# Performance work log

Hardware: AMD Instinct MI355X
Metric: run time of the kernel (lower is better)

The kernel has to match this reference:

```python
import jax, jax.numpy as jnp
import numpy as np

N = 100000      # nodes
E = 1600000     # edges (avg degree 16)
IN_FEATS = 128
HEADS = 4
OUT_FEATS = 16
NEG_SLOPE = 0.2
EPS = 1e-16


def setup_inputs() -> dict:
    key = jax.random.key(0)
    k1, k2, k3, k4, k5, k6 = jax.random.split(key, 6)
    feat = jax.random.normal(k1, (N, IN_FEATS), dtype=jnp.float32)
    # xavier-ish scale for params
    W = jax.random.normal(k2, (IN_FEATS, HEADS * OUT_FEATS), dtype=jnp.float32) * 0.1
    attn_l = jax.random.normal(k3, (1, HEADS, OUT_FEATS), dtype=jnp.float32) * 0.1
    attn_r = jax.random.normal(k4, (1, HEADS, OUT_FEATS), dtype=jnp.float32) * 0.1
    src_index = jax.random.randint(k5, (E,), 0, N, dtype=jnp.int32)
    trg_index = jax.random.randint(k6, (E,), 0, N, dtype=jnp.int32)
    return {"feat": feat, "W": W, "attn_l": attn_l, "attn_r": attn_r,
            "src_index": src_index, "trg_index": trg_index}


def reference(feat, W, attn_l, attn_r, src_index, trg_index):
    # dropout layers are identity in eval mode
    n = feat.shape[0]
    h = (feat @ W).reshape(n, HEADS, OUT_FEATS)            # [N,H,F]
    el = jnp.sum(h * attn_l, axis=-1)                      # [N,H]
    er = jnp.sum(h * attn_r, axis=-1)                      # [N,H]
    s = el[src_index] + er[trg_index]                      # [E,H] edge scores
    s = jnp.where(s > 0, s, NEG_SLOPE * s)                 # LeakyReLU(0.2)
    # neighborhood-aware softmax over incoming edges of each target node
    s = s - jnp.max(s)                                     # global max shift (as in source)
    e = jnp.exp(s)                                         # [E,H]
    denom = jax.ops.segment_sum(e, trg_index, num_segments=n)  # [N,H]
    attn = e / (denom[trg_index] + EPS)                    # [E,H]
    # weighted aggregation of lifted source features into target nodes
    msg = h[src_index] * attn[:, :, None]                  # [E,H,F]
    h_prime = jax.ops.segment_sum(msg, trg_index, num_segments=n)  # [N,H,F]
    return h_prime.reshape(n, HEADS * OUT_FEATS)
```

## Files before the change

kernel.cpp:

```cpp
#include <hip/hip_runtime.h>

typedef unsigned short ushort_t;
typedef __attribute__((ext_vector_type(8))) short bf16x8;
typedef __attribute__((ext_vector_type(4))) float f32x4v;

#define BN 128
#define LOGBN 7
#define CAP 3072
#define MAXBKT 1024
#define NB3 256

static __device__ __forceinline__ ushort_t f2bf(float f) {
  union { float f; unsigned int i; } v; v.f = f;
  unsigned int r = v.i + 0x7FFFu + ((v.i >> 16) & 1u);
  return (ushort_t)(r >> 16);
}
static __device__ __forceinline__ float leaky(float s) {
  return s > 0.f ? s : 0.2f * s;
}

__global__ __launch_bounds__(256) void packw_hist(
    const float* __restrict__ W, const float* __restrict__ attnl,
    const float* __restrict__ attnr, ushort_t* __restrict__ wfrag,
    const int* __restrict__ trg, int E, int nbkt,
    int* __restrict__ blockHist, int epb)
{
  const int b = blockIdx.x;
  const int t = threadIdx.x;
  if (b == NB3) {
    __shared__ float sW[128 * 64];
    __shared__ float sAl[64], sAr[64];
    for (int i = t; i < 128 * 64 / 4; i += 256)
      ((float4*)sW)[i] = ((const float4*)W)[i];
    if (t < 64) sAl[t] = attnl[t];
    else if (t < 128) sAr[t - 64] = attnr[t - 64];
    __syncthreads();
    const int kc = t >> 6, l = t & 63;
    const int q = l >> 4, n = l & 15;
    #pragma unroll
    for (int tile = 0; tile < 5; ++tile) {
      #pragma unroll
      for (int j = 0; j < 8; ++j) {
        const int k = kc * 32 + q * 8 + j;
        float v = 0.f;
        if (tile < 4) {
          v = sW[k * 64 + tile * 16 + n];
        } else if (n < 4) {
          for (int f = 0; f < 16; ++f)
            v += sW[k * 64 + n * 16 + f] * sAl[n * 16 + f];
        } else if (n < 8) {
          const int hd = n - 4;
          for (int f = 0; f < 16; ++f)
            v += sW[k * 64 + hd * 16 + f] * sAr[hd * 16 + f];
        }
        wfrag[((tile * 4 + kc) * 64 + l) * 8 + j] = f2bf(v);
      }
    }
    return;
  }
  __shared__ int hist[MAXBKT];
  for (int i = t; i < nbkt; i += 256) hist[i] = 0;
  __syncthreads();
  const int start = b * epb;
  const int end = min(start + epb, E);
  for (int e = start + t; e < end; e += 256)
    atomicAdd(&hist[trg[e] >> LOGBN], 1);
  __syncthreads();
  for (int i = t; i < nbkt; i += 256) blockHist[b * nbkt + i] = hist[i];
}

__global__ __launch_bounds__(256) void linear_scan(
    const float* __restrict__ feat, const ushort_t* __restrict__ wfrag,
    ushort_t* __restrict__ h_out, float* __restrict__ el, float* __restrict__ er,
    float* __restrict__ blockmax2, int N, int nbL,
    int* __restrict__ blockHist, int nbkt, int* __restrict__ colTotal)
{
  __shared__ ushort_t sFb[64 * 136];
  __shared__ float wmax[8];
  __shared__ int wt[4];
  const int t = threadIdx.x;
  const int b = blockIdx.x;
  const int w = t >> 6, l = t & 63;

  if (b >= nbL) {
    const int sb = b - nbL;
    const int v = blockHist[t * nbkt + sb];
    int incl = v;
    #pragma unroll
    for (int d = 1; d < 64; d <<= 1) {
      int u = __shfl_up(incl, d, 64);
      if (l >= d) incl += u;
    }
    if (l == 63) wt[w] = incl;
    __syncthreads();
    int woff = 0;
    for (int k = 0; k < w; ++k) woff += wt[k];
    blockHist[t * nbkt + sb] = woff + incl - v;
    if (t == 255) colTotal[sb] = woff + incl;
    return;
  }

  const int q = l >> 4, m = l & 15;
  const float4* gF = (const float4*)(feat + (size_t)b * 64 * 128);
  #pragma unroll
  for (int i = 0; i < 8; ++i) {
    const int idx = i * 256 + t;
    const int node = idx >> 5, off = idx & 31;
    float4 v = make_float4(0.f, 0.f, 0.f, 0.f);
    if (b * 64 + node < N) v = gF[idx];
    unsigned int p0 = ((unsigned int)f2bf(v.y) << 16) | f2bf(v.x);
    unsigned int p1 = ((unsigned int)f2bf(v.w) << 16) | f2bf(v.z);
    *(uint2*)(sFb + node * 136 + off * 4) = make_uint2(p0, p1);
  }
  __syncthreads();

  bf16x8 a[4];
  const ushort_t* arow = sFb + (w * 16 + m) * 136 + q * 8;
  #pragma unroll
  for (int kc = 0; kc < 4; ++kc)
    a[kc] = *(const bf16x8*)(arow + kc * 32);

  #pragma unroll
  for (int tile = 0; tile < 4; ++tile) {
    f32x4v acc = {0.f, 0.f, 0.f, 0.f};
    #pragma unroll
    for (int kc = 0; kc < 4; ++kc) {
      bf16x8 bfr = *(const bf16x8*)(wfrag + ((tile * 4 + kc) * 64 + l) * 8);
      acc = __builtin_amdgcn_mfma_f32_16x16x32_bf16(a[kc], bfr, acc, 0, 0, 0);
    }
    #pragma unroll
    for (int r = 0; r < 4; ++r) {
      const int gn = b * 64 + w * 16 + q * 4 + r;
      if (gn < N) h_out[(size_t)gn * 64 + tile * 16 + m] = f2bf(acc[r]);
    }
  }

  f32x4v acc4 = {0.f, 0.f, 0.f, 0.f};
  #pragma unroll
  for (int kc = 0; kc < 4; ++kc) {
    bf16x8 bfr = *(const bf16x8*)(wfrag + ((4 * 4 + kc) * 64 + l) * 8);
    acc4 = __builtin_amdgcn_mfma_f32_16x16x32_bf16(a[kc], bfr, acc4, 0, 0, 0);
  }
  float mel = -1e30f, mer = -1e30f;
  #pragma unroll
  for (int r = 0; r < 4; ++r) {
    const int gn = b * 64 + w * 16 + q * 4 + r;
    const float v = acc4[r];
    if (m < 4) {
      if (gn < N) el[gn * 4 + m] = v;
      mel = fmaxf(mel, v);
    } else if (m < 8) {
      if (gn < N) er[gn * 4 + (m - 4)] = v;
      mer = fmaxf(mer, v);
    }
  }
  #pragma unroll
  for (int o = 1; o <= 32; o <<= 1) {
    mel = fmaxf(mel, __shfl_xor(mel, o, 64));
    mer = fmaxf(mer, __shfl_xor(mer, o, 64));
  }
  if (l == 0) { wmax[w * 2] = mel; wmax[w * 2 + 1] = mer; }
  __syncthreads();
  if (t == 0) {
    float aa = fmaxf(fmaxf(wmax[0], wmax[2]), fmaxf(wmax[4], wmax[6]));
    float cc = fmaxf(fmaxf(wmax[1], wmax[3]), fmaxf(wmax[5], wmax[7]));
    blockmax2[b * 2] = aa;
    blockmax2[b * 2 + 1] = cc;
  }
}

__global__ __launch_bounds__(256) void bucket_scatter(
    const int* __restrict__ src, const int* __restrict__ trg, int E, int nbkt,
    const int* __restrict__ blockHist, const int* __restrict__ colTotal,
    unsigned int* __restrict__ binned, int epb, int* __restrict__ bucketBase)
{
  __shared__ int cursor[MAXBKT];
  __shared__ int wt[4];
  const int t = threadIdx.x, b = blockIdx.x;
  const int l = t & 63, w = t >> 6;

  int carry = 0;
  for (int ch = 0; ch * 256 < nbkt; ++ch) {
    const int i = ch * 256 + t;
    const int v = (i < nbkt) ? colTotal[i] : 0;
    int incl = v;
    #pragma unroll
    for (int d = 1; d < 64; d <<= 1) {
      int u = __shfl_up(incl, d, 64);
      if (l >= d) incl += u;
    }
    if (l == 63) wt[w] = incl;
    __syncthreads();
    int woff = 0;
    for (int k = 0; k < w; ++k) woff += wt[k];
    if (i < nbkt) cursor[i] = carry + woff + incl - v;
    carry += wt[0] + wt[1] + wt[2] + wt[3];
    __syncthreads();
  }
  if (b == 0) {
    for (int i = t; i < nbkt; i += 256) bucketBase[i] = cursor[i];
    if (t == 0) bucketBase[nbkt] = carry;
  }
  for (int i = t; i < nbkt; i += 256) cursor[i] += blockHist[b * nbkt + i];
  __syncthreads();

  const int start = b * epb;
  const int end = min(start + epb, E);
  for (int e = start + t; e < end; e += 256) {
    const int ti = trg[e];
    const int bkt = ti >> LOGBN;
    const int pos = atomicAdd(&cursor[bkt], 1);
    binned[pos] = ((unsigned int)src[e] << LOGBN) | (unsigned int)(ti & (BN - 1));
  }
}

__global__ __launch_bounds__(256) void fine_sort(
    unsigned int* __restrict__ binned, const int* __restrict__ bucketBase,
    int* __restrict__ rowbeg, int* __restrict__ rowend, int N,
    const float* __restrict__ blockmax2, int nbL, float* __restrict__ gmaxM)
{
  __shared__ unsigned int pld[CAP];
  __shared__ int hist[BN];
  __shared__ int cursor[BN];
  __shared__ int wtot[2];
  __shared__ float wmg[8];
  const int t = threadIdx.x;
  const int b = blockIdx.x;
  const int base = bucketBase[b];
  const int cn = min(bucketBase[b + 1] - base, CAP);
  unsigned int* slot = binned + base;

  if (t < BN) hist[t] = 0;
  if (b == 0) {
    const int l = t & 63, w = t >> 6;
    float mel = -1e30f, mer = -1e30f;
    for (int i = t; i < nbL; i += 256) {
      mel = fmaxf(mel, blockmax2[i * 2]);
      mer = fmaxf(mer, blockmax2[i * 2 + 1]);
    }
    #pragma unroll
    for (int o = 1; o <= 32; o <<= 1) {
      mel = fmaxf(mel, __shfl_xor(mel, o, 64));
      mer = fmaxf(mer, __shfl_xor(mer, o, 64));
    }
    if (l == 0) { wmg[w * 2] = mel; wmg[w * 2 + 1] = mer; }
  }
  __syncthreads();
  if (b == 0 && t == 0) {
    float aa = fmaxf(fmaxf(wmg[0], wmg[2]), fmaxf(wmg[4], wmg[6]));
    float cc = fmaxf(fmaxf(wmg[1], wmg[3]), fmaxf(wmg[5], wmg[7]));
    gmaxM[0] = fmaxf(0.f, aa + cc);
  }
  for (int i = t; i < cn; i += 256) {
    const unsigned int pv = slot[i];
    pld[i] = pv;
    atomicAdd(&hist[pv & (BN - 1)], 1);
  }
  __syncthreads();

  int v = 0, incl = 0;
  if (t < BN) {
    v = hist[t];
    incl = v;
    #pragma unroll
    for (int d = 1; d < 64; d <<= 1) {
      int u = __shfl_up(incl, d, 64);
      if ((t & 63) >= d) incl += u;
    }
  }
  if (t < BN && (t & 63) == 63) wtot[t >> 6] = incl;
  __syncthreads();
  if (t < BN) {
    const int excl = incl - v + ((t >= 64) ? wtot[0] : 0);
    cursor[t] = excl;
    const int node = b * BN + t;
    if (node < N) {
      rowbeg[node] = base + excl;
      rowend[node] = base + excl + v;
    }
  }
  __syncthreads();

  for (int i = t; i < cn; i += 256) {
    const unsigned int pv = pld[i];
    const int pos = atomicAdd(&cursor[pv & (BN - 1)], 1);
    slot[pos] = pv >> LOGBN;
  }
}

#define UNPACK_FMA(hv, p, acc) do { \
  union { unsigned int i; float f; } c_; \
  c_.i = (hv).x << 16;          acc[0] += c_.f * (p); \
  c_.i = (hv).x & 0xffff0000u;  acc[1] += c_.f * (p); \
  c_.i = (hv).y << 16;          acc[2] += c_.f * (p); \
  c_.i = (hv).y & 0xffff0000u;  acc[3] += c_.f * (p); \
  c_.i = (hv).z << 16;          acc[4] += c_.f * (p); \
  c_.i = (hv).z & 0xffff0000u;  acc[5] += c_.f * (p); \
  c_.i = (hv).w << 16;          acc[6] += c_.f * (p); \
  c_.i = (hv).w & 0xffff0000u;  acc[7] += c_.f * (p); \
} while (0)

#define LOADJ(j, hA_, hB_, qA_, qB_) do { \
  const int i_ = iA0 + (j) * 4; \
  const int sA_ = sSw[i_]; \
  const int sB_ = sSw[i_ + 32]; \
  qA_ = sPw[i_ * 4 + hd2]; \
  qB_ = sPw[(i_ + 32) * 4 + hd2]; \
  hA_ = *(const uint4*)(hcg + (size_t)sA_ * 64); \
  hB_ = *(const uint4*)(hcg + (size_t)sB_ * 64); \
} while (0)

__global__ __launch_bounds__(256) void gat_agg(
    const unsigned int* __restrict__ csrsrc, const int* __restrict__ rowbeg,
    const int* __restrict__ rowend,
    const float4* __restrict__ el4, const float4* __restrict__ er4,
    const ushort_t* __restrict__ hbf, const float* __restrict__ gmaxM,
    float* __restrict__ out, int N)
{
  __shared__ float sP[4 * 64 * 4];
  __shared__ int sS[4 * 64];
  const int t = threadIdx.x;
  const int l = t & 63;
  const int w = t >> 6;
  const int nbase = blockIdx.x * 16 + w * 4;
  const int rg = l >> 3;
  const int cg = l & 7;
  const int hd2 = cg >> 1;
  const int ks = l >> 4;
  const int le = l & 15;
  const float M = gmaxM[0];
  float* sPw = sP + w * 256;
  int* sSw = sS + w * 64;
  const ushort_t* hcg = hbf + cg * 8;
  const int iA0 = ((rg >> 2) * 16) + (rg & 3);

  const int nk = nbase + ks;
  int rs = 0, re = 0;
  if (nk < N) { rs = rowbeg[nk]; re = rowend[nk]; }
  const float4 ernk = (rs < re) ? er4[nk]
                                : make_float4(0.f, 0.f, 0.f, 0.f);
  int deg = re - rs;
  deg = max(deg, __shfl_xor(deg, 16, 64));
  deg = max(deg, __shfl_xor(deg, 32, 64));
  const int chunks = (deg + 15) >> 4;

  float aA[8] = {0.f,0.f,0.f,0.f,0.f,0.f,0.f,0.f};
  float aB[8] = {0.f,0.f,0.f,0.f,0.f,0.f,0.f,0.f};
  float dA = 0.f, dB = 0.f;

  for (int c = 0; c < chunks; ++c) {
    int sn = 0;
    float4 pv = make_float4(0.f, 0.f, 0.f, 0.f);
    const int ei = rs + c * 16 + le;
    if (ei < re) {
      sn = (int)csrsrc[ei];
      const float4 a = el4[sn];
      pv.x = __expf(leaky(a.x + ernk.x) - M);
      pv.y = __expf(leaky(a.y + ernk.y) - M);
      pv.z = __expf(leaky(a.z + ernk.z) - M);
      pv.w = __expf(leaky(a.w + ernk.w) - M);
    }
    *(float4*)(sPw + l * 4) = pv;
    sSw[l] = sn;

    const int rem = min(deg - c * 16, 16);
    const int jmax = (rem + 3) >> 2;
    uint4 h0A, h0B, h1A, h1B, h2A, h2B, h3A, h3B;
    float q0A, q0B, q1A, q1B, q2A, q2B, q3A, q3B;
    LOADJ(0, h0A, h0B, q0A, q0B);
    if (jmax > 1) LOADJ(1, h1A, h1B, q1A, q1B);
    if (jmax > 2) LOADJ(2, h2A, h2B, q2A, q2B);
    if (jmax > 3) LOADJ(3, h3A, h3B, q3A, q3B);

    UNPACK_FMA(h0A, q0A, aA); UNPACK_FMA(h0B, q0B, aB);
    dA += q0A; dB += q0B;
    if (jmax > 1) {
      UNPACK_FMA(h1A, q1A, aA); UNPACK_FMA(h1B, q1B, aB);
      dA += q1A; dB += q1B;
    }
    if (jmax > 2) {
      UNPACK_FMA(h2A, q2A, aA); UNPACK_FMA(h2B, q2B, aB);
      dA += q2A; dB += q2B;
    }
    if (jmax > 3) {
      UNPACK_FMA(h3A, q3A, aA); UNPACK_FMA(h3B, q3B, aB);
      dA += q3A; dB += q3B;
    }
  }

  #pragma unroll
  for (int o = 8; o <= 16; o <<= 1) {
    #pragma unroll
    for (int i = 0; i < 8; ++i) {
      aA[i] += __shfl_xor(aA[i], o, 64);
      aB[i] += __shfl_xor(aB[i], o, 64);
    }
    dA += __shfl_xor(dA, o, 64);
    dB += __shfl_xor(dB, o, 64);
  }
  if ((rg & 3) == 0) {
    const int nA = nbase + (rg >> 2);
    const int nB = nA + 2;
    const float rA = 1.0f / (dA + 1e-16f);
    const float rB = 1.0f / (dB + 1e-16f);
    if (nA < N) {
      float4* orow = (float4*)(out + (size_t)nA * 64 + cg * 8);
      orow[0] = make_float4(aA[0] * rA, aA[1] * rA, aA[2] * rA, aA[3] * rA);
      orow[1] = make_float4(aA[4] * rA, aA[5] * rA, aA[6] * rA, aA[7] * rA);
    }
    if (nB < N) {
      float4* orow = (float4*)(out + (size_t)nB * 64 + cg * 8);
      orow[0] = make_float4(aB[0] * rB, aB[1] * rB, aB[2] * rB, aB[3] * rB);
      orow[1] = make_float4(aB[4] * rB, aB[5] * rB, aB[6] * rB, aB[7] * rB);
    }
  }
}

extern "C" void kernel_launch(void* const* d_in, const int* in_sizes, int n_in,
                              void* d_out, int out_size, void* d_ws, size_t ws_size,
                              hipStream_t stream) {
  const float* feat  = (const float*)d_in[0];
  const float* W     = (const float*)d_in[1];
  const float* attnl = (const float*)d_in[2];
  const float* attnr = (const float*)d_in[3];
  const int* src = (const int*)d_in[4];
  const int* trg = (const int*)d_in[5];
  float* out = (float*)d_out;

  const int N = in_sizes[0] / 128;
  const int E = in_sizes[4];

  const int nbL  = (N + 63) / 64;
  const int nbkt = (N + BN - 1) >> LOGBN;
  const int epb  = (E + NB3 - 1) / NB3;

  char* p = (char*)d_ws;
  auto take = [&](size_t bytes) -> char* {
    char* r = p;
    p += (bytes + 255) & ~(size_t)255;
    return r;
  };
  ushort_t* h_bf  = (ushort_t*)take((size_t)N * 64 * 2);
  float* el       = (float*)take((size_t)N * 16);
  float* er       = (float*)take((size_t)N * 16);
  unsigned int* binned = (unsigned int*)take((size_t)E * 4);
  int* rowbeg     = (int*)take((size_t)N * 4);
  int* rowend     = (int*)take((size_t)N * 4);
  ushort_t* wfrag = (ushort_t*)take(5 * 4 * 64 * 8 * 2);
  int* blockHist  = (int*)take((size_t)NB3 * nbkt * 4);
  int* colTotal   = (int*)take((size_t)nbkt * 4);
  int* bucketBase = (int*)take((size_t)(nbkt + 1) * 4);
  float* blockmax2 = (float*)take((size_t)nbL * 2 * 4);
  float* gmaxM    = (float*)take(256);

  packw_hist<<<NB3 + 1, 256, 0, stream>>>(W, attnl, attnr, wfrag,
                                          trg, E, nbkt, blockHist, epb);
  linear_scan<<<nbL + nbkt, 256, 0, stream>>>(feat, wfrag, h_bf, el, er,
                                              blockmax2, N, nbL,
                                              blockHist, nbkt, colTotal);
  bucket_scatter<<<NB3, 256, 0, stream>>>(src, trg, E, nbkt, blockHist,
                                          colTotal, binned, epb, bucketBase);
  fine_sort<<<nbkt, 256, 0, stream>>>(binned, bucketBase, rowbeg, rowend, N,
                                      blockmax2, nbL, gmaxM);
  gat_agg<<<(N + 15) / 16, 256, 0, stream>>>(binned, rowbeg, rowend,
                                             (const float4*)el,
                                             (const float4*)er, h_bf,
                                             gmaxM, out, N);
}
```

Before: 210.1 us.

## Fuse preprocessing kernels into one cooperative persistent kernel with grid syncs

Merges the weight-pack/histogram, linear/scan, bucket scatter and fine sort kernels into a single cooperative kernel, with grid.sync between phases and a shared-memory union. Linear-transform tiles are pulled dynamically from an atomic counter so idle blocks overlap that work with the scan and scatter phases. The aim is to remove kernel launch gaps and tail effects across four launches. In exchange it adds grid-wide barriers, a memset and an occupancy query, and the large shared union may limit occupancy.

```diff
diff --git a/kernel.cpp b/kernel.cpp
--- a/kernel.cpp
+++ b/kernel.cpp
@@ -1,4 +1,7 @@
 #include <hip/hip_runtime.h>
+#include <hip/hip_cooperative_groups.h>
+
+namespace cg = cooperative_groups;
 
 typedef unsigned short ushort_t;
 typedef __attribute__((ext_vector_type(8))) short bf16x8;
@@ -19,88 +22,16 @@
   return s > 0.f ? s : 0.2f * s;
 }
 
-__global__ __launch_bounds__(256) void packw_hist(
-    const float* __restrict__ W, const float* __restrict__ attnl,
-    const float* __restrict__ attnr, ushort_t* __restrict__ wfrag,
-    const int* __restrict__ trg, int E, int nbkt,
-    int* __restrict__ blockHist, int epb)
+static __device__ void linear_unit(
+    int b, const float* __restrict__ feat, const ushort_t* __restrict__ wfrag,
+    ushort_t* __restrict__ h_out, float* __restrict__ el,
+    float* __restrict__ er, float* __restrict__ blockmax2, int N,
+    ushort_t* sFb, float* wmax)
 {
-  const int b = blockIdx.x;
   const int t = threadIdx.x;
-  if (b == NB3) {
-    __shared__ float sW[128 * 64];
-    __shared__ float sAl[64], sAr[64];
-    for (int i = t; i < 128 * 64 / 4; i += 256)
-      ((float4*)sW)[i] = ((const float4*)W)[i];
-    if (t < 64) sAl[t] = attnl[t];
-    else if (t < 128) sAr[t - 64] = attnr[t - 64];
-    __syncthreads();
-    const int kc = t >> 6, l = t & 63;
-    const int q = l >> 4, n = l & 15;
-    #pragma unroll
-    for (int tile = 0; tile < 5; ++tile) {
-      #pragma unroll
-      for (int j = 0; j < 8; ++j) {
-        const int k = kc * 32 + q * 8 + j;
-        float v = 0.f;
-        if (tile < 4) {
-          v = sW[k * 64 + tile * 16 + n];
-        } else if (n < 4) {
-          for (int f = 0; f < 16; ++f)
-            v += sW[k * 64 + n * 16 + f] * sAl[n * 16 + f];
-        } else if (n < 8) {
-          const int hd = n - 4;
-          for (int f = 0; f < 16; ++f)
-            v += sW[k * 64 + hd * 16 + f] * sAr[hd * 16 + f];
-        }
-        wfrag[((tile * 4 + kc) * 64 + l) * 8 + j] = f2bf(v);
-      }
-    }
-    return;
-  }
-  __shared__ int hist[MAXBKT];
-  for (int i = t; i < nbkt; i += 256) hist[i] = 0;
+  const int w = t >> 6, l = t & 63;
+  const int q = l >> 4, m = l & 15;
   __syncthreads();
-  const int start = b * epb;
-  const int end = min(start + epb, E);
-  for (int e = start + t; e < end; e += 256)
-    atomicAdd(&hist[trg[e] >> LOGBN], 1);
-  __syncthreads();
-  for (int i = t; i < nbkt; i += 256) blockHist[b * nbkt + i] = hist[i];
-}
-
-__global__ __launch_bounds__(256) void linear_scan(
-    const float* __restrict__ feat, const ushort_t* __restrict__ wfrag,
-    ushort_t* __restrict__ h_out, float* __restrict__ el, float* __restrict__ er,
-    float* __restrict__ blockmax2, int N, int nbL,
-    int* __restrict__ blockHist, int nbkt, int* __restrict__ colTotal)
-{
-  __shared__ ushort_t sFb[64 * 136];
-  __shared__ float wmax[8];
-  __shared__ int wt[4];
-  const int t = threadIdx.x;
-  const int b = blockIdx.x;
-  const int w = t >> 6, l = t & 63;
-
-  if (b >= nbL) {
-    const int sb = b - nbL;
-    const int v = blockHist[t * nbkt + sb];
-    int incl = v;
-    #pragma unroll
-    for (int d = 1; d < 64; d <<= 1) {
-      int u = __shfl_up(incl, d, 64);
-      if (l >= d) incl += u;
-    }
-    if (l == 63) wt[w] = incl;
-    __syncthreads();
-    int woff = 0;
-    for (int k = 0; k < w; ++k) woff += wt[k];
-    blockHist[t * nbkt + sb] = woff + incl - v;
-    if (t == 255) colTotal[sb] = woff + incl;
-    return;
-  }
-
-  const int q = l >> 4, m = l & 15;
   const float4* gF = (const float4*)(feat + (size_t)b * 64 * 128);
   #pragma unroll
   for (int i = 0; i < 8; ++i) {
@@ -169,70 +100,196 @@
   }
 }
 
-__global__ __launch_bounds__(256) void bucket_scatter(
-    const int* __restrict__ src, const int* __restrict__ trg, int E, int nbkt,
-    const int* __restrict__ blockHist, const int* __restrict__ colTotal,
-    unsigned int* __restrict__ binned, int epb, int* __restrict__ bucketBase)
+static __device__ int pull_unit(int* linCtr, int nbL, int* pick) {
+  __syncthreads();
+  if (threadIdx.x == 0) *pick = atomicAdd(linCtr, 1);
+  __syncthreads();
+  return (*pick < nbL) ? *pick : -1;
+}
+
+__global__ __launch_bounds__(256) void gat_pre(
+    const float* __restrict__ W, const float* __restrict__ attnl,
+    const float* __restrict__ attnr, ushort_t* __restrict__ wfrag,
+    const int* __restrict__ src, const int* __restrict__ trg, int E,
+    int nbkt, int* __restrict__ blockHist, int epb,
+    const float* __restrict__ feat, ushort_t* __restrict__ h_bf,
+    float* __restrict__ el, float* __restrict__ er,
+    float* __restrict__ blockmax2, int N, int nbL,
+    int* __restrict__ colTotal, int* __restrict__ bucketBase,
+    unsigned int* __restrict__ binned,
+    int* __restrict__ rowbeg, int* __restrict__ rowend,
+    float* __restrict__ gmaxM, int* __restrict__ linCtr)
 {
-  __shared__ int cursor[MAXBKT];
-  __shared__ int wt[4];
-  const int t = threadIdx.x, b = blockIdx.x;
-  const int l = t & 63, w = t >> 6;
-
-  int carry = 0;
-  for (int ch = 0; ch * 256 < nbkt; ++ch) {
-    const int i = ch * 256 + t;
-    const int v = (i < nbkt) ? colTotal[i] : 0;
+  cg::grid_group grid = cg::this_grid();
+  const int gb = blockIdx.x;
+  const int G  = gridDim.x;
+  const int t  = threadIdx.x;
+  const int l  = t & 63, w = t >> 6;
+
+  __shared__ __align__(16) union {
+    struct { ushort_t sFb[64 * 136]; float wmax[8]; } lin;
+    int hist[MAXBKT];
+    struct { int cur[MAXBKT]; int wt[4]; } sc;
+    struct { unsigned int pld[CAP]; int h[BN]; int c[BN]; int wtot[2]; } fs;
+    float wmg[8];
+  } u;
+  __shared__ int pick;
+
+  const int stride = G >> 8;
+
+  const bool isHist = (gb % stride == 0) && (gb / stride < NB3);
+  if (isHist) {
+    const int hb = gb / stride;
+    for (int i = t; i < nbkt; i += 256) u.hist[i] = 0;
+    __syncthreads();
+    const int s0 = hb * epb, e0 = min(s0 + epb, E);
+    for (int e = s0 + t; e < e0; e += 256)
+      atomicAdd(&u.hist[trg[e] >> LOGBN], 1);
+    __syncthreads();
+    for (int i = t; i < nbkt; i += 256) blockHist[hb * nbkt + i] = u.hist[i];
+  }
+  if (gb == G - 1) {
+    const int kc = t >> 6;
+    const int q = l >> 4, n = l & 15;
+    #pragma unroll
+    for (int tile = 0; tile < 5; ++tile) {
+      #pragma unroll
+      for (int j = 0; j < 8; ++j) {
+        const int k = kc * 32 + q * 8 + j;
+        float v = 0.f;
+        if (tile < 4) {
+          v = W[k * 64 + tile * 16 + n];
+        } else if (n < 4) {
+          for (int f = 0; f < 16; ++f)
+            v += W[k * 64 + n * 16 + f] * attnl[n * 16 + f];
+        } else if (n < 8) {
+          const int hd = n - 4;
+          for (int f = 0; f < 16; ++f)
+            v += W[k * 64 + hd * 16 + f] * attnr[hd * 16 + f];
+        }
+        wfrag[((tile * 4 + kc) * 64 + l) * 8 + j] = f2bf(v);
+      }
+    }
+  }
+  __threadfence();
+  grid.sync();
+
+  for (int sb = gb; sb < nbkt; sb += G) {
+    const int v = blockHist[t * nbkt + sb];
     int incl = v;
     #pragma unroll
     for (int d = 1; d < 64; d <<= 1) {
-      int u = __shfl_up(incl, d, 64);
-      if (l >= d) incl += u;
-    }
-    if (l == 63) wt[w] = incl;
+      int uu = __shfl_up(incl, d, 64);
+      if (l >= d) incl += uu;
+    }
+    if (l == 63) u.sc.wt[w] = incl;
     __syncthreads();
     int woff = 0;
-    for (int k = 0; k < w; ++k) woff += wt[k];
-    if (i < nbkt) cursor[i] = carry + woff + incl - v;
-    carry += wt[0] + wt[1] + wt[2] + wt[3];
-    __syncthreads();
-  }
-  if (b == 0) {
-    for (int i = t; i < nbkt; i += 256) bucketBase[i] = cursor[i];
-    if (t == 0) bucketBase[nbkt] = carry;
-  }
-  for (int i = t; i < nbkt; i += 256) cursor[i] += blockHist[b * nbkt + i];
-  __syncthreads();
-
-  const int start = b * epb;
-  const int end = min(start + epb, E);
-  for (int e = start + t; e < end; e += 256) {
-    const int ti = trg[e];
-    const int bkt = ti >> LOGBN;
-    const int pos = atomicAdd(&cursor[bkt], 1);
-    binned[pos] = ((unsigned int)src[e] << LOGBN) | (unsigned int)(ti & (BN - 1));
-  }
-}
-
-__global__ __launch_bounds__(256) void fine_sort(
-    unsigned int* __restrict__ binned, const int* __restrict__ bucketBase,
-    int* __restrict__ rowbeg, int* __restrict__ rowend, int N,
-    const float* __restrict__ blockmax2, int nbL, float* __restrict__ gmaxM)
-{
-  __shared__ unsigned int pld[CAP];
-  __shared__ int hist[BN];
-  __shared__ int cursor[BN];
-  __shared__ int wtot[2];
-  __shared__ float wmg[8];
-  const int t = threadIdx.x;
-  const int b = blockIdx.x;
-  const int base = bucketBase[b];
-  const int cn = min(bucketBase[b + 1] - base, CAP);
-  unsigned int* slot = binned + base;
-
-  if (t < BN) hist[t] = 0;
-  if (b == 0) {
-    const int l = t & 63, w = t >> 6;
+    for (int k = 0; k < w; ++k) woff += u.sc.wt[k];
+    blockHist[t * nbkt + sb] = woff + incl - v;
+    if (t == 255) colTotal[sb] = woff + incl;
+    __syncthreads();
+  }
+  #pragma unroll 1
+  for (int qn = 0; qn < 2; ++qn) {
+    const int un = pull_unit(linCtr, nbL, &pick);
+    if (un < 0) break;
+    linear_unit(un, feat, wfrag, h_bf, el, er, blockmax2, N,
+                u.lin.sFb, u.lin.wmax);
+  }
+  __threadfence();
+  grid.sync();
+
+  const bool isScat = (gb % stride == 0) && (gb / stride < NB3);
+  if (isScat) {
+    const int sb2 = gb / stride;
+    int carry = 0;
+    for (int ch = 0; ch * 256 < nbkt; ++ch) {
+      const int i = ch * 256 + t;
+      const int v = (i < nbkt) ? colTotal[i] : 0;
+      int incl = v;
+      #pragma unroll
+      for (int d = 1; d < 64; d <<= 1) {
+        int uu = __shfl_up(incl, d, 64);
+        if (l >= d) incl += uu;
+      }
+      if (l == 63) u.sc.wt[w] = incl;
+      __syncthreads();
+      int woff = 0;
+      for (int k = 0; k < w; ++k) woff += u.sc.wt[k];
+      if (i < nbkt) u.sc.cur[i] = carry + woff + incl - v;
+      carry += u.sc.wt[0] + u.sc.wt[1] + u.sc.wt[2] + u.sc.wt[3];
+      __syncthreads();
+    }
+    if (gb == 0) {
+      for (int i = t; i < nbkt; i += 256) bucketBase[i] = u.sc.cur[i];
+      if (t == 0) bucketBase[nbkt] = carry;
+    }
+    for (int i = t; i < nbkt; i += 256) u.sc.cur[i] += blockHist[sb2 * nbkt + i];
+    __syncthreads();
+    const int s0 = sb2 * epb, e0 = min(s0 + epb, E);
+    for (int e = s0 + t; e < e0; e += 256) {
+      const int ti = trg[e];
+      const int bkt = ti >> LOGBN;
+      const int pos = atomicAdd(&u.sc.cur[bkt], 1);
+      binned[pos] = ((unsigned int)src[e] << LOGBN) | (unsigned int)(ti & (BN - 1));
+    }
+  } else {
+    #pragma unroll 1
+    while (true) {
+      const int un = pull_unit(linCtr, nbL, &pick);
+      if (un < 0) break;
+      linear_unit(un, feat, wfrag, h_bf, el, er, blockmax2, N,
+                  u.lin.sFb, u.lin.wmax);
+    }
+  }
+  __threadfence();
+  grid.sync();
+
+  #pragma unroll 1
+  for (int fb = gb; fb < nbkt; fb += G) {
+    __syncthreads();
+    const int base = bucketBase[fb];
+    const int cn = min(bucketBase[fb + 1] - base, CAP);
+    unsigned int* slot = binned + base;
+    if (t < BN) u.fs.h[t] = 0;
+    __syncthreads();
+    for (int i = t; i < cn; i += 256) {
+      const unsigned int pv = slot[i];
+      u.fs.pld[i] = pv;
+      atomicAdd(&u.fs.h[pv & (BN - 1)], 1);
+    }
+    __syncthreads();
+    int v = 0, incl = 0;
+    if (t < BN) {
+      v = u.fs.h[t];
+      incl = v;
+      #pragma unroll
+      for (int d = 1; d < 64; d <<= 1) {
+        int uu = __shfl_up(incl, d, 64);
+        if (l >= d) incl += uu;
+      }
+    }
+    if (t < BN && l == 63) u.fs.wtot[t >> 6] = incl;
+    __syncthreads();
+    if (t < BN) {
+      const int excl = incl - v + ((t >= 64) ? u.fs.wtot[0] : 0);
+      u.fs.c[t] = excl;
+      const int node = fb * BN + t;
+      if (node < N) {
+        rowbeg[node] = base + excl;
+        rowend[node] = base + excl + v;
+      }
+    }
+    __syncthreads();
+    for (int i = t; i < cn; i += 256) {
+      const unsigned int pv = u.fs.pld[i];
+      const int pos = atomicAdd(&u.fs.c[pv & (BN - 1)], 1);
+      slot[pos] = pv >> LOGBN;
+    }
+  }
+  if (gb == G - 1) {
+    __syncthreads();
     float mel = -1e30f, mer = -1e30f;
     for (int i = t; i < nbL; i += 256) {
       mel = fmaxf(mel, blockmax2[i * 2]);
@@ -243,48 +300,13 @@
       mel = fmaxf(mel, __shfl_xor(mel, o, 64));
       mer = fmaxf(mer, __shfl_xor(mer, o, 64));
     }
-    if (l == 0) { wmg[w * 2] = mel; wmg[w * 2 + 1] = mer; }
-  }
-  __syncthreads();
-  if (b == 0 && t == 0) {
-    float aa = fmaxf(fmaxf(wmg[0], wmg[2]), fmaxf(wmg[4], wmg[6]));
-    float cc = fmaxf(fmaxf(wmg[1], wmg[3]), fmaxf(wmg[5], wmg[7]));
-    gmaxM[0] = fmaxf(0.f, aa + cc);
-  }
-  for (int i = t; i < cn; i += 256) {
-    const unsigned int pv = slot[i];
-    pld[i] = pv;
-    atomicAdd(&hist[pv & (BN - 1)], 1);
-  }
-  __syncthreads();
-
-  int v = 0, incl = 0;
-  if (t < BN) {
-    v = hist[t];
-    incl = v;
-    #pragma unroll
-    for (int d = 1; d < 64; d <<= 1) {
-      int u = __shfl_up(incl, d, 64);
-      if ((t & 63) >= d) incl += u;
-    }
-  }
-  if (t < BN && (t & 63) == 63) wtot[t >> 6] = incl;
-  __syncthreads();
-  if (t < BN) {
-    const int excl = incl - v + ((t >= 64) ? wtot[0] : 0);
-    cursor[t] = excl;
-    const int node = b * BN + t;
-    if (node < N) {
-      rowbeg[node] = base + excl;
-      rowend[node] = base + excl + v;
-    }
-  }
-  __syncthreads();
-
-  for (int i = t; i < cn; i += 256) {
-    const unsigned int pv = pld[i];
-    const int pos = atomicAdd(&cursor[pv & (BN - 1)], 1);
-    slot[pos] = pv >> LOGBN;
+    if (l == 0) { u.wmg[w * 2] = mel; u.wmg[w * 2 + 1] = mer; }
+    __syncthreads();
+    if (t == 0) {
+      float aa = fmaxf(fmaxf(u.wmg[0], u.wmg[2]), fmaxf(u.wmg[4], u.wmg[6]));
+      float cc = fmaxf(fmaxf(u.wmg[1], u.wmg[3]), fmaxf(u.wmg[5], u.wmg[7]));
+      gmaxM[0] = fmaxf(0.f, aa + cc);
+    }
   }
 }
 
@@ -324,14 +346,14 @@
   const int w = t >> 6;
   const int nbase = blockIdx.x * 16 + w * 4;
   const int rg = l >> 3;
-  const int cg = l & 7;
-  const int hd2 = cg >> 1;
+  const int cg2 = l & 7;
+  const int hd2 = cg2 >> 1;
   const int ks = l >> 4;
   const int le = l & 15;
   const float M = gmaxM[0];
   float* sPw = sP + w * 256;
   int* sSw = sS + w * 64;
-  const ushort_t* hcg = hbf + cg * 8;
+  const ushort_t* hcg = hbf + cg2 * 8;
   const int iA0 = ((rg >> 2) * 16) + (rg & 3);
 
   const int nk = nbase + ks;
@@ -404,12 +426,12 @@
     const float rA = 1.0f / (dA + 1e-16f);
     const float rB = 1.0f / (dB + 1e-16f);
     if (nA < N) {
-      float4* orow = (float4*)(out + (size_t)nA * 64 + cg * 8);
+      float4* orow = (float4*)(out + (size_t)nA * 64 + cg2 * 8);
       orow[0] = make_float4(aA[0] * rA, aA[1] * rA, aA[2] * rA, aA[3] * rA);
       orow[1] = make_float4(aA[4] * rA, aA[5] * rA, aA[6] * rA, aA[7] * rA);
     }
     if (nB < N) {
-      float4* orow = (float4*)(out + (size_t)nB * 64 + cg * 8);
+      float4* orow = (float4*)(out + (size_t)nB * 64 + cg2 * 8);
       orow[0] = make_float4(aB[0] * rB, aB[1] * rB, aB[2] * rB, aB[3] * rB);
       orow[1] = make_float4(aB[4] * rB, aB[5] * rB, aB[6] * rB, aB[7] * rB);
     }
@@ -452,16 +474,27 @@
   int* bucketBase = (int*)take((size_t)(nbkt + 1) * 4);
   float* blockmax2 = (float*)take((size_t)nbL * 2 * 4);
   float* gmaxM    = (float*)take(256);
-
-  packw_hist<<<NB3 + 1, 256, 0, stream>>>(W, attnl, attnr, wfrag,
-                                          trg, E, nbkt, blockHist, epb);
-  linear_scan<<<nbL + nbkt, 256, 0, stream>>>(feat, wfrag, h_bf, el, er,
-                                              blockmax2, N, nbL,
-                                              blockHist, nbkt, colTotal);
-  bucket_scatter<<<NB3, 256, 0, stream>>>(src, trg, E, nbkt, blockHist,
-                                          colTotal, binned, epb, bucketBase);
-  fine_sort<<<nbkt, 256, 0, stream>>>(binned, bucketBase, rowbeg, rowend, N,
-                                      blockmax2, nbL, gmaxM);
+  int* linCtr     = (int*)take(256);
+
+  int maxb = 0;
+  hipOccupancyMaxActiveBlocksPerMultiprocessor(&maxb, gat_pre, 256, 0);
+  if (maxb < 1) maxb = 1;
+  if (maxb > 4) maxb = 4;
+  const int G = maxb * 256;
+
+  hipMemsetAsync(linCtr, 0, 4, stream);
+
+  void* args[] = {
+    (void*)&W, (void*)&attnl, (void*)&attnr, (void*)&wfrag,
+    (void*)&src, (void*)&trg, (void*)&E,
+    (void*)&nbkt, (void*)&blockHist, (void*)&epb,
+    (void*)&feat, (void*)&h_bf, (void*)&el, (void*)&er,
+    (void*)&blockmax2, (void*)&N, (void*)&nbL,
+    (void*)&colTotal, (void*)&bucketBase, (void*)&binned,
+    (void*)&rowbeg, (void*)&rowend, (void*)&gmaxM, (void*)&linCtr
+  };
+  hipLaunchCooperativeKernel(gat_pre, dim3(G), dim3(256), args, 0, stream);
+
   gat_agg<<<(N + 15) / 16, 256, 0, stream>>>(binned, rowbeg, rowend,
                                              (const float4*)el,
                                              (const float4*)er, h_bf,
```

New measurement: 699.9 us. 233% more time.
